# Optimization experiments

Hardware: AMD Instinct MI355X
Metric: run time of the kernel (lower is better)

## Reference

```python
import jax, jax.numpy as jnp
import numpy as np

# Dims: N tokens, D input, H expert hidden, O output, E experts, G gate hidden, K top-k
N, D, H, O, E, G, K = 8192, 1024, 2048, 1024, 8, 256, 2
BALANCE_COEF = 0.01


def setup_inputs() -> dict:
    key = jax.random.key(0)
    ks = jax.random.split(key, 12)
    def lin(k, shape, fan_in):
        return jax.random.normal(k, shape, jnp.float32) * (1.0 / np.sqrt(fan_in))
    return {
        "x":   jax.random.normal(ks[0], (N, D), jnp.float32),
        # gating MLP: D -> G -> E
        "Wg1": lin(ks[1], (D, G), D), "bg1": jnp.zeros((G,), jnp.float32),
        "Wg2": lin(ks[2], (G, E), G), "bg2": jnp.zeros((E,), jnp.float32),
        # stacked expert MLPs: D -> H -> H -> O (ExpertNetwork, num_layers=2)
        "W1": lin(ks[3], (E, D, H), D), "b1": jnp.zeros((E, H), jnp.float32),
        "W2": lin(ks[4], (E, H, H), H), "b2": jnp.zeros((E, H), jnp.float32),
        "W3": lin(ks[5], (E, H, O), H), "b3": jnp.zeros((E, O), jnp.float32),
    }


def reference(x, Wg1, bg1, Wg2, bg2, W1, b1, W2, b2, W3, b3):
    # Gating: 2-layer MLP -> softmax -> top-k -> renormalize (eval: no noise/dropout)
    logits = jnp.maximum(x @ Wg1 + bg1, 0.0) @ Wg2 + bg2            # [N, E]
    probs = jax.nn.softmax(logits, axis=-1)
    w, idx = jax.lax.top_k(probs, K)                                # [N, K]
    w = w / jnp.sum(w, axis=-1, keepdims=True)
    onehot = jax.nn.one_hot(idx, E, dtype=x.dtype)                  # [N, K, E]
    comb = jnp.sum(onehot * w[..., None], axis=1)                   # [N, E] per-token expert weight

    # Dense-equivalent combine: unselected tokens get weight 0, identical math to
    # the masked dispatch + scatter-add in the torch code.
    def expert_step(acc, params):
        W1e, b1e, W2e, b2e, W3e, b3e, we = params                   # we: [N]
        h = jnp.maximum(x @ W1e + b1e, 0.0)                         # [N, H]
        h = jnp.maximum(h @ W2e + b2e, 0.0)                         # [N, H]
        o = h @ W3e + b3e                                           # [N, O]
        return acc + o * we[:, None], None

    out, _ = jax.lax.scan(expert_step, jnp.zeros((N, O), x.dtype),
                          (W1, b1, W2, b2, W3, b3, comb.T))

    # aux losses: expert_usage[e] = sum_i mean_b(indices[b,i]==e)
    expert_usage = jnp.sum(onehot, axis=(0, 1)) / N                 # [E]
    balance_loss = jnp.mean((expert_usage - 1.0 / E) ** 2) * BALANCE_COEF
    return out, balance_loss, expert_usage
```

## Files before the change

### kernel.cpp

```cpp
#include <hip/hip_runtime.h>
#include <hip/hip_bf16.h>
#include <cstdint>
#include <cstddef>

#define N_TOK 8192
#define D_IN  1024
#define H_DIM 2048
#define O_DIM 1024
#define E_NUM 8
#define G_DIM 256
#define MAXTILES 136
#define MAXROWS  (MAXTILES*128)

typedef __attribute__((ext_vector_type(8))) __bf16 bf16x8;
typedef __attribute__((ext_vector_type(4))) float floatx4;

#define GCAST(p) ((__attribute__((address_space(1))) void*)(void*)(p))
#define LCAST(p) ((__attribute__((address_space(3))) void*)(p))

#define JOB_G1_END   512
#define JOB_CAST_END 4608
#define JOB_W1_END   8704

__device__ inline void transpose_body(const float* __restrict__ src,
                                      __bf16* __restrict__ dst,
                                      int K, int N, int e, int ktile, int ntile,
                                      float* smemf) {
  float (*tl)[64] = (float(*)[64])smemf;
  const float* s = src + (size_t)e * K * N;
  __bf16* d = dst + (size_t)e * K * N;
  int k0 = ktile * 64, n0 = ntile * 64;
  int t = threadIdx.x;
  int kr = t >> 4, nc = t & 15;
#pragma unroll
  for (int p = 0; p < 4; p++) {
    int r = kr + p * 16;
    float4 v = *reinterpret_cast<const float4*>(
        s + (size_t)(k0 + r) * N + n0 + nc * 4);
    *reinterpret_cast<float4*>(&tl[r][(nc * 4 + 8 * (r >> 3)) & 63]) = v;
  }
  __syncthreads();
  int n = t >> 3, kg = t & 7;
#pragma unroll
  for (int p = 0; p < 2; p++) {
    int c = n + p * 32;
    bf16x8 o;
#pragma unroll
    for (int j = 0; j < 8; j++)
      o[j] = (__bf16)tl[kg * 8 + j][(c + 8 * kg) & 63];
    *reinterpret_cast<bf16x8*>(d + (size_t)(n0 + c) * K + k0 + kg * 8) = o;
  }
}

__device__ inline void gate1_body(const float* __restrict__ x,
                                  const float* __restrict__ Wg1,
                                  const float* __restrict__ bg1,
                                  float* __restrict__ g,
                                  int bn, int bm, float* smemf) {
  float (*As)[68] = (float(*)[68])smemf;
  float (*Bs)[68] = (float(*)[68])(smemf + 32 * 68);
  int t = threadIdx.x;
  int tm = t >> 4, tn = t & 15;
  float acc[4][4] = {};
  for (int k0 = 0; k0 < D_IN; k0 += 32) {
#pragma unroll
    for (int i = 0; i < 2; i++) {
      int idx = t + 256 * i;
      int row = idx >> 3, c4 = idx & 7;
      float4 v = *reinterpret_cast<const float4*>(
          x + (size_t)(bm * 64 + row) * D_IN + k0 + c4 * 4);
      As[c4 * 4 + 0][row] = v.x;
      As[c4 * 4 + 1][row] = v.y;
      As[c4 * 4 + 2][row] = v.z;
      As[c4 * 4 + 3][row] = v.w;
      int brow = idx >> 4, bc4 = idx & 15;
      float4 wv = *reinterpret_cast<const float4*>(
          Wg1 + (size_t)(k0 + brow) * G_DIM + bn * 64 + bc4 * 4);
      *reinterpret_cast<float4*>(&Bs[brow][bc4 * 4]) = wv;
    }
    __syncthreads();
#pragma unroll
    for (int k = 0; k < 32; k++) {
      float4 av = *reinterpret_cast<const float4*>(&As[k][tm * 4]);
      float4 bv = *reinterpret_cast<const float4*>(&Bs[k][tn * 4]);
      float a4[4] = {av.x, av.y, av.z, av.w};
      float b4[4] = {bv.x, bv.y, bv.z, bv.w};
#pragma unroll
      for (int r = 0; r < 4; r++)
#pragma unroll
        for (int c = 0; c < 4; c++) acc[r][c] = fmaf(a4[r], b4[c], acc[r][c]);
    }
    __syncthreads();
  }
  int gr = bm * 64 + tm * 4, gc = bn * 64 + tn * 4;
#pragma unroll
  for (int r = 0; r < 4; r++) {
    float4 o;
    o.x = fmaxf(acc[r][0] + bg1[gc + 0], 0.f);
    o.y = fmaxf(acc[r][1] + bg1[gc + 1], 0.f);
    o.z = fmaxf(acc[r][2] + bg1[gc + 2], 0.f);
    o.w = fmaxf(acc[r][3] + bg1[gc + 3], 0.f);
    *reinterpret_cast<float4*>(g + (size_t)(gr + r) * G_DIM + gc) = o;
  }
}

__global__ __launch_bounds__(256) void prep_kernel(
    const float* __restrict__ x, __bf16* __restrict__ xb,
    const float* __restrict__ W1, __bf16* __restrict__ W1t,
    const float* __restrict__ Wg1, const float* __restrict__ bg1,
    float* __restrict__ g) {
  __shared__ float smemf[4352];
  int b = blockIdx.x;
  if (b < JOB_G1_END) {
    gate1_body(x, Wg1, bg1, g, b & 3, b >> 2, smemf);
  } else if (b < JOB_CAST_END) {
    int id = b - JOB_G1_END;
    int i = id * 2048 + threadIdx.x * 8;
    float4 v0 = *reinterpret_cast<const float4*>(x + i);
    float4 v1 = *reinterpret_cast<const float4*>(x + i + 4);
    bf16x8 o;
    o[0] = (__bf16)v0.x; o[1] = (__bf16)v0.y; o[2] = (__bf16)v0.z; o[3] = (__bf16)v0.w;
    o[4] = (__bf16)v1.x; o[5] = (__bf16)v1.y; o[6] = (__bf16)v1.z; o[7] = (__bf16)v1.w;
    *reinterpret_cast<bf16x8*>(xb + i) = o;
  } else {
    int id = b - JOB_CAST_END;
    transpose_body(W1, W1t, D_IN, H_DIM, id >> 9, (id >> 5) & 15, id & 31, smemf);
  }
}

__global__ __launch_bounds__(256) void gate2_kernel(const float* __restrict__ g,
                                                    const float* __restrict__ Wg2,
                                                    const float* __restrict__ bg2,
                                                    int* __restrict__ top_idx,
                                                    float* __restrict__ top_w,
                                                    int* __restrict__ counts) {
  __shared__ float lg[32][9];
  int t = threadIdx.x;
  int tl = t >> 3, e = t & 7;
  int n = blockIdx.x * 32 + tl;
  const float* gr = g + (size_t)n * G_DIM;
  float acc = bg2[e];
  for (int i = 0; i < G_DIM; i += 4) {
    float4 v = *reinterpret_cast<const float4*>(gr + i);
    acc += v.x * Wg2[(i + 0) * E_NUM + e];
    acc += v.y * Wg2[(i + 1) * E_NUM + e];
    acc += v.z * Wg2[(i + 2) * E_NUM + e];
    acc += v.w * Wg2[(i + 3) * E_NUM + e];
  }
  lg[tl][e] = acc;
  __syncthreads();
  if (e == 0) {
    float l[8];
#pragma unroll
    for (int i = 0; i < 8; i++) l[i] = lg[tl][i];
    int i0 = 0;
    for (int i = 1; i < 8; i++)
      if (l[i] > l[i0]) i0 = i;
    int i1 = (i0 == 0) ? 1 : 0;
    for (int i = 0; i < 8; i++)
      if (i != i0 && l[i] > l[i1]) i1 = i;
    float d = expf(l[i1] - l[i0]);
    float w0 = 1.f / (1.f + d);
    float w1 = d * w0;
    top_idx[n * 2 + 0] = i0;
    top_idx[n * 2 + 1] = i1;
    top_w[n * 2 + 0] = w0;
    top_w[n * 2 + 1] = w1;
    atomicAdd(&counts[i0], 1);
    atomicAdd(&counts[i1], 1);
  }
}

__global__ void g3_kernel(const int* __restrict__ counts, int* __restrict__ cursors,
                          int* __restrict__ off_pad, int* __restrict__ ntiles,
                          int* __restrict__ tile_meta, float* __restrict__ out_tail,
                          int* __restrict__ slot_token) {
  if (threadIdx.x == 0) {
    int off = 0, nt = 0;
    float mse = 0.f;
    for (int e = 0; e < E_NUM; e++) {
      off_pad[e] = off;
      int c = counts[e];
      int tiles = (c + 127) >> 7;
      for (int i = 0; i < tiles; i++) {
        tile_meta[nt * 2 + 0] = e;
        tile_meta[nt * 2 + 1] = off + i * 128;
        nt++;
      }
      off += tiles << 7;
      cursors[e] = 0;
      float u = (float)c / (float)N_TOK;
      out_tail[1 + e] = u;
      float dd = u - 0.125f;
      mse += dd * dd;
    }
    *ntiles = nt;
    out_tail[0] = (mse / 8.0f) * 0.01f;
  }
  for (int s = threadIdx.x; s < MAXROWS; s += 256) slot_token[s] = 0;
}

__global__ __launch_bounds__(256) void scatter_kernel(const int* __restrict__ top_idx,
                                                      const int* __restrict__ off_pad,
                                                      int* __restrict__ cursors,
                                                      int* __restrict__ slot_token,
                                                      int* __restrict__ token_slots) {
  int n = blockIdx.x * 256 + threadIdx.x;
#pragma unroll
  for (int k = 0; k < 2; k++) {
    int e = top_idx[n * 2 + k];
    int pos = atomicAdd(&cursors[e], 1);
    int s = off_pad[e] + pos;
    slot_token[s] = n;
    token_slots[n * 2 + k] = s;
  }
}

__global__ __launch_bounds__(256) void moe_gemm_kernel(
    const __bf16* __restrict__ A, int Astride, int gatherA,
    const __bf16* __restrict__ Wt, const float* __restrict__ bias,
    int Kdim, int Ndim,
    const int* __restrict__ tile_meta, const int* __restrict__ ntiles_p,
    const int* __restrict__ slot_token,
    __bf16* __restrict__ h_out, float* __restrict__ y_out, int finalMode,
    const float* __restrict__ W2src, __bf16* __restrict__ W2dst,
    const float* __restrict__ W3src, __bf16* __restrict__ W3dst) {
  __shared__ __align__(16) char smem[32768];
  int tile = blockIdx.y;
  if (tile >= MAXTILES) {
    int id = (tile - MAXTILES) * gridDim.x + blockIdx.x;
    if (id < 8192) {
      transpose_body(W2src, W2dst, H_DIM, H_DIM, id >> 10, (id >> 5) & 31,
                     id & 31, (float*)smem);
    } else {
      id -= 8192;
      transpose_body(W3src, W3dst, H_DIM, O_DIM, id >> 9, (id >> 4) & 31,
                     id & 15, (float*)smem);
    }
    return;
  }
  if (tile >= *ntiles_p) return;
  __bf16* As = (__bf16*)smem;
  __bf16* Bs = (__bf16*)(smem + 16384);
  int ex = tile_meta[tile * 2 + 0];
  int slot0 = tile_meta[tile * 2 + 1];
  int n0 = blockIdx.x * 128;
  int t = threadIdx.x, l = t & 63, w = t >> 6;

  size_t aoff[4], boff[4];
#pragma unroll
  for (int i = 0; i < 4; i++) {
    int gidx = (w * 4 + i) * 64 + l;
    int row = gidx >> 3;
    int kch = (gidx & 7) ^ (row & 7);
    int sl = slot0 + row;
    long long rb = gatherA ? (long long)slot_token[sl] * Astride
                           : (long long)sl * Astride;
    aoff[i] = (size_t)rb + kch * 8;
    boff[i] = ((size_t)ex * Ndim + n0 + row) * (size_t)Kdim + kch * 8;
  }

  int wm = (w >> 1) * 64, wn = (w & 1) * 64;
  int lm = l & 15, lq = l >> 4;
  floatx4 acc[4][4] = {};

  for (int k0 = 0; k0 < Kdim; k0 += 64) {
#pragma unroll
    for (int i = 0; i < 4; i++) {
      __builtin_amdgcn_global_load_lds(GCAST(A + aoff[i] + k0),
                                       LCAST((char*)As + w * 4096 + i * 1024),
                                       16, 0, 0);
      __builtin_amdgcn_global_load_lds(GCAST(Wt + boff[i] + k0),
                                       LCAST((char*)Bs + w * 4096 + i * 1024),
                                       16, 0, 0);
    }
    __syncthreads();
#pragma unroll
    for (int half = 0; half < 2; half++) {
      bf16x8 af[4], bfr[4];
#pragma unroll
      for (int i = 0; i < 4; i++) {
        int r = wm + i * 16 + lm;
        int s = (half * 4 + lq) ^ (r & 7);
        af[i] = *reinterpret_cast<const bf16x8*>(As + r * 64 + s * 8);
      }
#pragma unroll
      for (int j = 0; j < 4; j++) {
        int r = wn + j * 16 + lm;
        int s = (half * 4 + lq) ^ (r & 7);
        bfr[j] = *reinterpret_cast<const bf16x8*>(Bs + r * 64 + s * 8);
      }
#pragma unroll
      for (int i = 0; i < 4; i++)
#pragma unroll
        for (int j = 0; j < 4; j++)
          acc[i][j] = __builtin_amdgcn_mfma_f32_16x16x32_bf16(af[i], bfr[j],
                                                              acc[i][j], 0, 0, 0);
    }
    __syncthreads();
  }

  float bcol[4];
#pragma unroll
  for (int j = 0; j < 4; j++) bcol[j] = bias[(size_t)ex * Ndim + n0 + wn + j * 16 + lm];

  if (finalMode) {
#pragma unroll
    for (int i = 0; i < 4; i++) {
#pragma unroll
      for (int r = 0; r < 4; r++) {
        int sl = slot0 + wm + i * 16 + lq * 4 + r;
        float* yrow = y_out + (size_t)sl * Ndim + n0 + wn + lm;
#pragma unroll
        for (int j = 0; j < 4; j++) yrow[j * 16] = acc[i][j][r] + bcol[j];
      }
    }
  } else {
#pragma unroll
    for (int i = 0; i < 4; i++) {
#pragma unroll
      for (int r = 0; r < 4; r++) {
        int sl = slot0 + wm + i * 16 + lq * 4 + r;
        __bf16* hrow = h_out + (size_t)sl * Ndim + n0 + wn + lm;
#pragma unroll
        for (int j = 0; j < 4; j++) {
          float v = fmaxf(acc[i][j][r] + bcol[j], 0.f);
          hrow[j * 16] = (__bf16)v;
        }
      }
    }
  }
}

__global__ __launch_bounds__(256) void combine_kernel(const float* __restrict__ y,
                                                      const int* __restrict__ token_slots,
                                                      const float* __restrict__ top_w,
                                                      float* __restrict__ out) {
  int n = blockIdx.x;
  int t = threadIdx.x;
  int s0 = token_slots[n * 2 + 0], s1 = token_slots[n * 2 + 1];
  float w0 = top_w[n * 2 + 0], w1 = top_w[n * 2 + 1];
  float4 a = reinterpret_cast<const float4*>(y + (size_t)s0 * O_DIM)[t];
  float4 b = reinterpret_cast<const float4*>(y + (size_t)s1 * O_DIM)[t];
  float4 o;
  o.x = w0 * a.x + w1 * b.x;
  o.y = w0 * a.y + w1 * b.y;
  o.z = w0 * a.z + w1 * b.z;
  o.w = w0 * a.w + w1 * b.w;
  reinterpret_cast<float4*>(out + (size_t)n * O_DIM)[t] = o;
}

extern "C" void kernel_launch(void* const* d_in, const int* in_sizes, int n_in,
                              void* d_out, int out_size, void* d_ws, size_t ws_size,
                              hipStream_t stream) {
  const float* x   = (const float*)d_in[0];
  const float* Wg1 = (const float*)d_in[1];
  const float* bg1 = (const float*)d_in[2];
  const float* Wg2 = (const float*)d_in[3];
  const float* bg2 = (const float*)d_in[4];
  const float* W1  = (const float*)d_in[5];
  const float* b1  = (const float*)d_in[6];
  const float* W2  = (const float*)d_in[7];
  const float* b2  = (const float*)d_in[8];
  const float* W3  = (const float*)d_in[9];
  const float* b3  = (const float*)d_in[10];
  float* out = (float*)d_out;

  char* ws = (char*)d_ws;
  __bf16* x_bf       = (__bf16*)(ws + 0);
  __bf16* W1t        = (__bf16*)(ws + 16777216);
  __bf16* W2t        = (__bf16*)(ws + 50331648);
  __bf16* W3t        = (__bf16*)(ws + 117440512);
  __bf16* h1         = (__bf16*)(ws + 150994944);
  __bf16* h2         = (__bf16*)(ws + 222298112);
  float*  y          = (float*) (ws + 150994944);
  float*  gbuf       = (float*) (ws + 293601280);
  int*    top_idx    = (int*)   (ws + 301989888);
  float*  top_w      = (float*) (ws + 302055424);
  int*    slot_token = (int*)   (ws + 302120960);
  int*    token_slots= (int*)   (ws + 302190592);
  int*    meta       = (int*)   (ws + 302260224);
  int* counts    = meta;
  int* cursors   = meta + 8;
  int* off_pad   = meta + 16;
  int* ntiles    = meta + 24;
  int* tile_meta = meta + 32;
  float* out_tail = out + (size_t)N_TOK * O_DIM;

  hipMemsetAsync(meta, 0, 64, stream);

  prep_kernel<<<JOB_W1_END, 256, 0, stream>>>(x, x_bf, W1, W1t, Wg1, bg1, gbuf);
  gate2_kernel<<<N_TOK / 32, 256, 0, stream>>>(gbuf, Wg2, bg2, top_idx, top_w, counts);
  g3_kernel<<<1, 256, 0, stream>>>(counts, cursors, off_pad, ntiles, tile_meta, out_tail,
                                   slot_token);
  scatter_kernel<<<N_TOK / 256, 256, 0, stream>>>(top_idx, off_pad, cursors,
                                                  slot_token, token_slots);

  moe_gemm_kernel<<<dim3(H_DIM / 128, MAXTILES + 768), 256, 0, stream>>>(
      x_bf, D_IN, 1, W1t, b1, D_IN, H_DIM, tile_meta, ntiles, slot_token,
      h1, nullptr, 0, W2, W2t, W3, W3t);
  moe_gemm_kernel<<<dim3(H_DIM / 128, MAXTILES), 256, 0, stream>>>(
      h1, H_DIM, 0, W2t, b2, H_DIM, H_DIM, tile_meta, ntiles, slot_token,
      h2, nullptr, 0, nullptr, nullptr, nullptr, nullptr);
  moe_gemm_kernel<<<dim3(O_DIM / 128, MAXTILES), 256, 0, stream>>>(
      h2, H_DIM, 0, W3t, b3, H_DIM, O_DIM, tile_meta, ntiles, slot_token,
      nullptr, y, 1, nullptr, nullptr, nullptr, nullptr);
  combine_kernel<<<N_TOK, 256, 0, stream>>>(y, token_slots, top_w, out);
}
```

Measured before the change: 944.6 us.

## Add 256x256-tile pipelined GEMM kernel for expert layers 2 and 3

```diff
diff --git a/kernel.cpp b/kernel.cpp
--- a/kernel.cpp
+++ b/kernel.cpp
@@ -9,8 +9,9 @@
 #define O_DIM 1024
 #define E_NUM 8
 #define G_DIM 256
-#define MAXTILES 136
-#define MAXROWS  (MAXTILES*128)
+#define MAXT256 72
+#define MAXT128 144
+#define MAXROWS (MAXT256*256)
 
 typedef __attribute__((ext_vector_type(8))) __bf16 bf16x8;
 typedef __attribute__((ext_vector_type(4))) float floatx4;
@@ -172,29 +173,33 @@
 }
 
 __global__ void g3_kernel(const int* __restrict__ counts, int* __restrict__ cursors,
-                          int* __restrict__ off_pad, int* __restrict__ ntiles,
-                          int* __restrict__ tile_meta, float* __restrict__ out_tail,
+                          int* __restrict__ off_pad, int* __restrict__ nt128,
+                          int* __restrict__ nt256,
+                          int* __restrict__ meta128, int* __restrict__ meta256,
+                          float* __restrict__ out_tail,
                           int* __restrict__ slot_token) {
   if (threadIdx.x == 0) {
-    int off = 0, nt = 0;
+    int off = 0, n2 = 0, n1 = 0;
     float mse = 0.f;
     for (int e = 0; e < E_NUM; e++) {
       off_pad[e] = off;
       int c = counts[e];
-      int tiles = (c + 127) >> 7;
+      int tiles = (c + 255) >> 8;
       for (int i = 0; i < tiles; i++) {
-        tile_meta[nt * 2 + 0] = e;
-        tile_meta[nt * 2 + 1] = off + i * 128;
-        nt++;
-      }
-      off += tiles << 7;
+        int s0 = off + i * 256;
+        meta256[n2 * 2 + 0] = e; meta256[n2 * 2 + 1] = s0; n2++;
+        meta128[n1 * 2 + 0] = e; meta128[n1 * 2 + 1] = s0; n1++;
+        meta128[n1 * 2 + 0] = e; meta128[n1 * 2 + 1] = s0 + 128; n1++;
+      }
+      off += tiles << 8;
       cursors[e] = 0;
       float u = (float)c / (float)N_TOK;
       out_tail[1 + e] = u;
       float dd = u - 0.125f;
       mse += dd * dd;
     }
-    *ntiles = nt;
+    *nt256 = n2;
+    *nt128 = n1;
     out_tail[0] = (mse / 8.0f) * 0.01f;
   }
   for (int s = threadIdx.x; s < MAXROWS; s += 256) slot_token[s] = 0;
@@ -217,18 +222,18 @@
 }
 
 __global__ __launch_bounds__(256) void moe_gemm_kernel(
-    const __bf16* __restrict__ A, int Astride, int gatherA,
+    const __bf16* __restrict__ A, int Astride,
     const __bf16* __restrict__ Wt, const float* __restrict__ bias,
     int Kdim, int Ndim,
     const int* __restrict__ tile_meta, const int* __restrict__ ntiles_p,
     const int* __restrict__ slot_token,
-    __bf16* __restrict__ h_out, float* __restrict__ y_out, int finalMode,
+    __bf16* __restrict__ h_out,
     const float* __restrict__ W2src, __bf16* __restrict__ W2dst,
     const float* __restrict__ W3src, __bf16* __restrict__ W3dst) {
   __shared__ __align__(16) char smem[32768];
   int tile = blockIdx.y;
-  if (tile >= MAXTILES) {
-    int id = (tile - MAXTILES) * gridDim.x + blockIdx.x;
+  if (tile >= MAXT128) {
+    int id = (tile - MAXT128) * gridDim.x + blockIdx.x;
     if (id < 8192) {
       transpose_body(W2src, W2dst, H_DIM, H_DIM, id >> 10, (id >> 5) & 31,
                      id & 31, (float*)smem);
@@ -254,8 +259,7 @@
     int row = gidx >> 3;
     int kch = (gidx & 7) ^ (row & 7);
     int sl = slot0 + row;
-    long long rb = gatherA ? (long long)slot_token[sl] * Astride
-                           : (long long)sl * Astride;
+    long long rb = (long long)slot_token[sl] * Astride;
     aoff[i] = (size_t)rb + kch * 8;
     boff[i] = ((size_t)ex * Ndim + n0 + row) * (size_t)Kdim + kch * 8;
   }
@@ -303,25 +307,197 @@
   float bcol[4];
 #pragma unroll
   for (int j = 0; j < 4; j++) bcol[j] = bias[(size_t)ex * Ndim + n0 + wn + j * 16 + lm];
+#pragma unroll
+  for (int i = 0; i < 4; i++) {
+#pragma unroll
+    for (int r = 0; r < 4; r++) {
+      int sl = slot0 + wm + i * 16 + lq * 4 + r;
+      __bf16* hrow = h_out + (size_t)sl * Ndim + n0 + wn + lm;
+#pragma unroll
+      for (int j = 0; j < 4; j++) {
+        float v = fmaxf(acc[i][j][r] + bcol[j], 0.f);
+        hrow[j * 16] = (__bf16)v;
+      }
+    }
+  }
+}
+
+__global__ __launch_bounds__(512) void moe_gemm256_kernel(
+    const __bf16* __restrict__ A,
+    const __bf16* __restrict__ Wt, const float* __restrict__ bias,
+    int Kdim, int Ndim,
+    const int* __restrict__ tile_meta, const int* __restrict__ ntiles_p,
+    __bf16* __restrict__ h_out, float* __restrict__ y_out, int finalMode) {
+  __shared__ __align__(16) char smem[131072];
+  int tile = blockIdx.y;
+  if (tile >= *ntiles_p) return;
+  int ex = tile_meta[tile * 2 + 0];
+  int slot0 = tile_meta[tile * 2 + 1];
+  int n0 = blockIdx.x * 256;
+  int t = threadIdx.x, l = t & 63, w = t >> 6;
+  int wm2 = w >> 2, wn4 = w & 3;
+  int lm = l & 15, lq = l >> 4;
+
+  size_t aoff[2][2], boff[2][2];
+#pragma unroll
+  for (int h = 0; h < 2; h++)
+#pragma unroll
+    for (int i = 0; i < 2; i++) {
+      int gidx = i * 512 + t;
+      int row = gidx >> 3;
+      int kch = (gidx & 7) ^ (row & 7);
+      aoff[h][i] = (size_t)(slot0 + h * 128 + row) * (size_t)Kdim + kch * 8;
+      boff[h][i] = ((size_t)ex * Ndim + n0 + h * 128 + row) * (size_t)Kdim + kch * 8;
+    }
+
+  floatx4 acc[8][4] = {};
+
+  auto SA = [&](int kt, int h, int d) {
+    char* dst = smem + d * 65536 + h * 16384;
+#pragma unroll
+    for (int i = 0; i < 2; i++)
+      __builtin_amdgcn_global_load_lds(GCAST(A + aoff[h][i] + (size_t)kt * 64),
+                                       LCAST(dst + i * 8192 + w * 1024), 16, 0, 0);
+  };
+  auto SB = [&](int kt, int h, int d) {
+    char* dst = smem + d * 65536 + 32768 + h * 16384;
+#pragma unroll
+    for (int i = 0; i < 2; i++)
+      __builtin_amdgcn_global_load_lds(GCAST(Wt + boff[h][i] + (size_t)kt * 64),
+                                       LCAST(dst + i * 8192 + w * 1024), 16, 0, 0);
+  };
+
+  int NKT = Kdim >> 6;
+  int NIT = NKT >> 1;
+
+  asm volatile("s_waitcnt vmcnt(0)" ::: "memory");
+  SA(0, 0, 0); SA(0, 1, 0); SB(0, 0, 0); SB(0, 1, 0);
+  SB(1, 0, 1); SB(1, 1, 1);
+  asm volatile("s_waitcnt vmcnt(4)" ::: "memory");
+  __builtin_amdgcn_s_barrier();
+  __builtin_amdgcn_sched_barrier(0);
+
+#pragma unroll 1
+  for (int it = 0; it < NIT; ++it) {
+    int kt1 = 2 * it + 1, kt2 = 2 * it + 2, kt3 = 2 * it + 3;
+    bool last = (it == NIT - 1);
+    bf16x8 bfr[4][2];
+
+#pragma unroll
+    for (int q = 0; q < 4; q++) {
+      bf16x8 af[2][2];
+      const __bf16* As = (const __bf16*)(smem);
+      const __bf16* Bsl = (const __bf16*)(smem + 32768);
+      if (q == 0) {
+#pragma unroll
+        for (int j = 0; j < 4; j++) {
+          int c = wn4 * 64 + j * 16 + lm;
+#pragma unroll
+          for (int ks = 0; ks < 2; ks++)
+            bfr[j][ks] = *reinterpret_cast<const bf16x8*>(Bsl + c * 64 + ((ks * 4 + lq) ^ (c & 7)) * 8);
+        }
+      }
+#pragma unroll
+      for (int ii = 0; ii < 2; ii++) {
+        int r = wm2 * 128 + (q * 2 + ii) * 16 + lm;
+#pragma unroll
+        for (int ks = 0; ks < 2; ks++)
+          af[ii][ks] = *reinterpret_cast<const bf16x8*>(As + r * 64 + ((ks * 4 + lq) ^ (r & 7)) * 8);
+      }
+      if (q == 0) SA(kt1, 0, 1);
+      else if (q == 1) SA(kt1, 1, 1);
+      else if (q == 2) { if (kt2 < NKT) SB(kt2, 0, 0); }
+      else             { if (kt2 < NKT) SB(kt2, 1, 0); }
+      __builtin_amdgcn_s_barrier();
+      asm volatile("s_waitcnt lgkmcnt(0)" ::: "memory");
+      __builtin_amdgcn_sched_barrier(0);
+      __builtin_amdgcn_s_setprio(1);
+#pragma unroll
+      for (int ii = 0; ii < 2; ii++)
+#pragma unroll
+        for (int j = 0; j < 4; j++)
+#pragma unroll
+          for (int ks = 0; ks < 2; ks++)
+            acc[q * 2 + ii][j] = __builtin_amdgcn_mfma_f32_16x16x32_bf16(
+                af[ii][ks], bfr[j][ks], acc[q * 2 + ii][j], 0, 0, 0);
+      __builtin_amdgcn_s_setprio(0);
+      if (q == 3) {
+        if (last) asm volatile("s_waitcnt vmcnt(0)" ::: "memory");
+        else      asm volatile("s_waitcnt vmcnt(4)" ::: "memory");
+      }
+      __builtin_amdgcn_s_barrier();
+      __builtin_amdgcn_sched_barrier(0);
+    }
+
+#pragma unroll
+    for (int q = 0; q < 4; q++) {
+      bf16x8 af[2][2];
+      const __bf16* As = (const __bf16*)(smem + 65536);
+      const __bf16* Bsl = (const __bf16*)(smem + 65536 + 32768);
+      if (q == 0) {
+#pragma unroll
+        for (int j = 0; j < 4; j++) {
+          int c = wn4 * 64 + j * 16 + lm;
+#pragma unroll
+          for (int ks = 0; ks < 2; ks++)
+            bfr[j][ks] = *reinterpret_cast<const bf16x8*>(Bsl + c * 64 + ((ks * 4 + lq) ^ (c & 7)) * 8);
+        }
+      }
+#pragma unroll
+      for (int ii = 0; ii < 2; ii++) {
+        int r = wm2 * 128 + (q * 2 + ii) * 16 + lm;
+#pragma unroll
+        for (int ks = 0; ks < 2; ks++)
+          af[ii][ks] = *reinterpret_cast<const bf16x8*>(As + r * 64 + ((ks * 4 + lq) ^ (r & 7)) * 8);
+      }
+      if (q == 0)      { if (kt2 < NKT) SA(kt2, 0, 0); }
+      else if (q == 1) { if (kt2 < NKT) SA(kt2, 1, 0); }
+      else if (q == 2) { if (kt3 < NKT) SB(kt3, 0, 1); }
+      else             { if (kt3 < NKT) SB(kt3, 1, 1); }
+      __builtin_amdgcn_s_barrier();
+      asm volatile("s_waitcnt lgkmcnt(0)" ::: "memory");
+      __builtin_amdgcn_sched_barrier(0);
+      __builtin_amdgcn_s_setprio(1);
+#pragma unroll
+      for (int ii = 0; ii < 2; ii++)
+#pragma unroll
+        for (int j = 0; j < 4; j++)
+#pragma unroll
+          for (int ks = 0; ks < 2; ks++)
+            acc[q * 2 + ii][j] = __builtin_amdgcn_mfma_f32_16x16x32_bf16(
+                af[ii][ks], bfr[j][ks], acc[q * 2 + ii][j], 0, 0, 0);
+      __builtin_amdgcn_s_setprio(0);
+      if (q == 3 && !last) {
+        asm volatile("s_waitcnt vmcnt(4)" ::: "memory");
+      }
+      __builtin_amdgcn_s_barrier();
+      __builtin_amdgcn_sched_barrier(0);
+    }
+  }
+
+  float bcol[4];
+#pragma unroll
+  for (int j = 0; j < 4; j++)
+    bcol[j] = bias[(size_t)ex * Ndim + n0 + wn4 * 64 + j * 16 + lm];
 
   if (finalMode) {
 #pragma unroll
-    for (int i = 0; i < 4; i++) {
+    for (int i = 0; i < 8; i++) {
 #pragma unroll
       for (int r = 0; r < 4; r++) {
-        int sl = slot0 + wm + i * 16 + lq * 4 + r;
-        float* yrow = y_out + (size_t)sl * Ndim + n0 + wn + lm;
+        int sl = slot0 + wm2 * 128 + i * 16 + lq * 4 + r;
+        float* yrow = y_out + (size_t)sl * Ndim + n0 + wn4 * 64 + lm;
 #pragma unroll
         for (int j = 0; j < 4; j++) yrow[j * 16] = acc[i][j][r] + bcol[j];
       }
     }
   } else {
 #pragma unroll
-    for (int i = 0; i < 4; i++) {
+    for (int i = 0; i < 8; i++) {
 #pragma unroll
       for (int r = 0; r < 4; r++) {
-        int sl = slot0 + wm + i * 16 + lq * 4 + r;
-        __bf16* hrow = h_out + (size_t)sl * Ndim + n0 + wn + lm;
+        int sl = slot0 + wm2 * 128 + i * 16 + lq * 4 + r;
+        __bf16* hrow = h_out + (size_t)sl * Ndim + n0 + wn4 * 64 + lm;
 #pragma unroll
         for (int j = 0; j < 4; j++) {
           float v = fmaxf(acc[i][j][r] + bcol[j], 0.f);
@@ -372,38 +548,38 @@
   __bf16* W2t        = (__bf16*)(ws + 50331648);
   __bf16* W3t        = (__bf16*)(ws + 117440512);
   __bf16* h1         = (__bf16*)(ws + 150994944);
-  __bf16* h2         = (__bf16*)(ws + 222298112);
-  float*  y          = (float*) (ws + 150994944);
-  float*  gbuf       = (float*) (ws + 293601280);
+  __bf16* h2         = (__bf16*)(ws + 226492416);
+  float*  y          = (float*) (ws + 16777216);
+  float*  gbuf       = (float*) (ws + 226492416);
   int*    top_idx    = (int*)   (ws + 301989888);
   float*  top_w      = (float*) (ws + 302055424);
   int*    slot_token = (int*)   (ws + 302120960);
-  int*    token_slots= (int*)   (ws + 302190592);
+  int*    token_slots= (int*)   (ws + 302194688);
   int*    meta       = (int*)   (ws + 302260224);
   int* counts    = meta;
   int* cursors   = meta + 8;
   int* off_pad   = meta + 16;
-  int* ntiles    = meta + 24;
-  int* tile_meta = meta + 32;
+  int* nt128     = meta + 24;
+  int* nt256     = meta + 25;
+  int* meta128   = meta + 32;
+  int* meta256   = meta + 320;
   float* out_tail = out + (size_t)N_TOK * O_DIM;
 
   hipMemsetAsync(meta, 0, 64, stream);
 
   prep_kernel<<<JOB_W1_END, 256, 0, stream>>>(x, x_bf, W1, W1t, Wg1, bg1, gbuf);
   gate2_kernel<<<N_TOK / 32, 256, 0, stream>>>(gbuf, Wg2, bg2, top_idx, top_w, counts);
-  g3_kernel<<<1, 256, 0, stream>>>(counts, cursors, off_pad, ntiles, tile_meta, out_tail,
-                                   slot_token);
+  g3_kernel<<<1, 256, 0, stream>>>(counts, cursors, off_pad, nt128, nt256,
+                                   meta128, meta256, out_tail, slot_token);
   scatter_kernel<<<N_TOK / 256, 256, 0, stream>>>(top_idx, off_pad, cursors,
                                                   slot_token, token_slots);
 
-  moe_gemm_kernel<<<dim3(H_DIM / 128, MAXTILES + 768), 256, 0, stream>>>(
-      x_bf, D_IN, 1, W1t, b1, D_IN, H_DIM, tile_meta, ntiles, slot_token,
-      h1, nullptr, 0, W2, W2t, W3, W3t);
-  moe_gemm_kernel<<<dim3(H_DIM / 128, MAXTILES), 256, 0, stream>>>(
-      h1, H_DIM, 0, W2t, b2, H_DIM, H_DIM, tile_meta, ntiles, slot_token,
-      h2, nullptr, 0, nullptr, nullptr, nullptr, nullptr);
-  moe_gemm_kernel<<<dim3(O_DIM / 128, MAXTILES), 256, 0, stream>>>(
-      h2, H_DIM, 0, W3t, b3, H_DIM, O_DIM, tile_meta, ntiles, slot_token,
-      nullptr, y, 1, nullptr, nullptr, nullptr, nullptr);
+  moe_gemm_kernel<<<dim3(H_DIM / 128, MAXT128 + 768), 256, 0, stream>>>(
+      x_bf, D_IN, W1t, b1, D_IN, H_DIM, meta128, nt128, slot_token,
+      h1, W2, W2t, W3, W3t);
+  moe_gemm256_kernel<<<dim3(H_DIM / 256, MAXT256), 512, 0, stream>>>(
+      h1, W2t, b2, H_DIM, H_DIM, meta256, nt256, h2, nullptr, 0);
+  moe_gemm256_kernel<<<dim3(O_DIM / 256, MAXT256), 512, 0, stream>>>(
+      h2, W3t, b3, H_DIM, O_DIM, meta256, nt256, nullptr, y, 1);
   combine_kernel<<<N_TOK, 256, 0, stream>>>(y, token_slots, top_w, out);
 }
```

New measurement: 975.9 us. 3.3% more time.
